# Optimization experiments

Measured on AMD Instinct MI355X. Metric: run time of the kernel, lower is better.

Reference implementation:

```python
import jax, jax.numpy as jnp
import numpy as np

K_HOPS = 2


def setup_inputs() -> dict:
    key = jax.random.key(0)
    k1, k2, k3 = jax.random.split(key, 3)
    N, E, D, C = 100000, 3200000, 512, 40
    x = jax.random.normal(k1, (N, D), dtype=jnp.float32)
    edge_index = jax.random.randint(k2, (2, E), 0, N, dtype=jnp.int64)
    W = jax.random.normal(k3, (C, D), dtype=jnp.float32) * 0.05
    b = jnp.zeros((C,), dtype=jnp.float32)
    return {"x": x, "edge_index": edge_index, "W": W, "b": b}


def reference(x, edge_index, W, b):
    # SGConv: K-hop symmetric-normalized propagation, then Linear, then log_softmax.
    # Dropout is identity at inference (training=False).
    N = x.shape[0]
    loop = jnp.arange(N, dtype=edge_index.dtype)
    src = jnp.concatenate([edge_index[0], loop])  # source nodes (+ self-loops)
    dst = jnp.concatenate([edge_index[1], loop])  # target nodes (+ self-loops)
    ew = jnp.ones(src.shape[0], dtype=x.dtype)
    # deg^{-1/2} A_hat deg^{-1/2}: degree computed at the target (col) index, as in PyG gcn_norm
    deg = jax.ops.segment_sum(ew, dst, num_segments=N)
    dinv = jnp.where(deg > 0, jax.lax.rsqrt(deg), 0.0)
    norm = dinv[src] * dinv[dst]  # [E+N]
    h = x
    for _ in range(K_HOPS):
        # gather source features, weight, scatter-add to targets
        h = jax.ops.segment_sum(norm[:, None] * h[src], dst, num_segments=N)
    logits = h @ W.T + b  # [N, C]
    return jax.nn.log_softmax(logits, axis=1)
```

## Files before the change

### kernel.cpp

```cpp
#include <hip/hip_runtime.h>
#include <hip/hip_bf16.h>


#define TPB 256
#define ETILE 16384
#define ZS 64

typedef __attribute__((ext_vector_type(8))) short short8v;
typedef __attribute__((ext_vector_type(4))) float f32x4;

__device__ inline short f2bf(float f) {
    unsigned u = __float_as_uint(f);
    unsigned r = (u + 0x7fffu + ((u >> 16) & 1u)) >> 16;
    return (short)r;
}
__device__ inline float bf2f(short s) {
    return __uint_as_float(((unsigned)(unsigned short)s) << 16);
}

__global__ void k_wconv(const float* __restrict__ W, short* __restrict__ Wb,
                        int* __restrict__ bcnt, int nb) {
    if (blockIdx.x == 0)
        for (int i = threadIdx.x; i < nb; i += TPB) bcnt[i] = 0;
    int idx = blockIdx.x * TPB + threadIdx.x;
    int c = idx >> 9, k = idx & 511;
    float v = (c < 40) ? W[c * 512 + k] : 0.f;
    Wb[idx] = f2bf(v);
}

__global__ __launch_bounds__(TPB) void k_bhist(
    const int* __restrict__ dst, int* __restrict__ bcnt, int E, int nb) {
    __shared__ int h[512];
    int t = threadIdx.x;
    for (int i = t; i < nb; i += TPB) h[i] = 0;
    __syncthreads();
    int e0 = blockIdx.x * ETILE;
    int e1 = min(e0 + ETILE, E);
    for (int e = e0 + t; e < e1; e += TPB)
        atomicAdd(&h[dst[e] >> 8], 1);
    __syncthreads();
    for (int i = t; i < nb; i += TPB)
        if (h[i]) atomicAdd(&bcnt[i], h[i]);
}

__global__ __launch_bounds__(512) void k_boff(
    const int* __restrict__ bcnt, int* __restrict__ boff,
    int* __restrict__ bcur, int nb) {
    __shared__ int s[512];
    int t = threadIdx.x;
    int own = (t < nb) ? bcnt[t] : 0;
    s[t] = own;
    __syncthreads();
    for (int off = 1; off < 512; off <<= 1) {
        int v = (t >= off) ? s[t - off] : 0;
        __syncthreads();
        s[t] += v;
        __syncthreads();
    }
    if (t < nb) {
        int ex = s[t] - own;
        boff[t] = ex;
        bcur[t] = ex;
        if (t == nb - 1) boff[nb] = s[t];
    }
}

__global__ __launch_bounds__(TPB) void k_part(
    const int* __restrict__ src, const int* __restrict__ dst,
    int* __restrict__ bcur, int* __restrict__ pairs, int E, int nb) {
    __shared__ int hist[512], base[512];
    int t = threadIdx.x;
    for (int i = t; i < nb; i += TPB) hist[i] = 0;
    __syncthreads();
    int e0 = blockIdx.x * ETILE;
    int e1 = min(e0 + ETILE, E);
    for (int e = e0 + t; e < e1; e += TPB)
        atomicAdd(&hist[dst[e] >> 8], 1);
    __syncthreads();
    for (int i = t; i < nb; i += TPB) {
        base[i] = hist[i] ? atomicAdd(&bcur[i], hist[i]) : 0;
        hist[i] = 0;
    }
    __syncthreads();
    for (int e = e0 + t; e < e1; e += TPB) {
        int d = dst[e];
        int b = d >> 8;
        int pos = base[b] + atomicAdd(&hist[b], 1);
        pairs[pos] = ((d & 255) << 20) | src[e];
    }
}

__global__ __launch_bounds__(TPB) void k_sort(
    const int* __restrict__ pairs, const int* __restrict__ boff,
    int* __restrict__ csr, int* __restrict__ row_ptr, float* __restrict__ dinv,
    int N, int nb) {
    __shared__ int hist[256], excl[256], lcur[256];
    int b = blockIdx.x, t = threadIdx.x;
    hist[t] = 0;
    __syncthreads();
    int beg = boff[b], end = boff[b + 1];
    for (int j = beg + t; j < end; j += TPB)
        atomicAdd(&hist[pairs[j] >> 20], 1);
    __syncthreads();
    int own = hist[t];
    excl[t] = own;
    __syncthreads();
    for (int off = 1; off < 256; off <<= 1) {
        int v = (t >= off) ? excl[t - off] : 0;
        __syncthreads();
        excl[t] += v;
        __syncthreads();
    }
    int node = (b << 8) + t;
    if (node < N) {
        row_ptr[node] = beg + excl[t] - own;
        dinv[node] = rsqrtf((float)(own + 1));
    }
    lcur[t] = 0;
    __syncthreads();
    for (int j = beg + t; j < end; j += TPB) {
        int u = pairs[j];
        int dl = u >> 20;
        int pos = beg + (excl[dl] - hist[dl]) + atomicAdd(&lcur[dl], 1);
        csr[pos] = u & 0xFFFFF;
    }
    if (b == nb - 1 && t == 0) row_ptr[N] = end;
}

__global__ __launch_bounds__(TPB) void k_matmul_mfma(
    const float* __restrict__ x, const short* __restrict__ Wb,
    const float* __restrict__ dinv, short* __restrict__ z, int N) {
    int wid  = threadIdx.x >> 6;
    int lane = threadIdx.x & 63;
    int rbase = blockIdx.x * 64 + wid * 16;
    if (rbase >= N) return;
    int arow   = rbase + (lane & 15);
    int aclamp = min(arow, N - 1);
    int koff   = (lane >> 4) * 8;
    const float* xrow = x + (size_t)aclamp * 512 + koff;
    const short* wb   = Wb + (lane & 15) * 512 + koff;

    f32x4 acc0 = {0.f,0.f,0.f,0.f}, acc1 = {0.f,0.f,0.f,0.f}, acc2 = {0.f,0.f,0.f,0.f};
    for (int ks = 0; ks < 16; ++ks) {
        int k0 = ks * 32;
        float4 f0 = *reinterpret_cast<const float4*>(xrow + k0);
        float4 f1 = *reinterpret_cast<const float4*>(xrow + k0 + 4);
        short8v a;
        a[0] = f2bf(f0.x); a[1] = f2bf(f0.y); a[2] = f2bf(f0.z); a[3] = f2bf(f0.w);
        a[4] = f2bf(f1.x); a[5] = f2bf(f1.y); a[6] = f2bf(f1.z); a[7] = f2bf(f1.w);
        short8v b0 = *reinterpret_cast<const short8v*>(wb + k0);
        short8v b1 = *reinterpret_cast<const short8v*>(wb + 16 * 512 + k0);
        short8v b2 = *reinterpret_cast<const short8v*>(wb + 32 * 512 + k0);
        acc0 = __builtin_amdgcn_mfma_f32_16x16x32_bf16(a, b0, acc0, 0, 0, 0);
        acc1 = __builtin_amdgcn_mfma_f32_16x16x32_bf16(a, b1, acc1, 0, 0, 0);
        acc2 = __builtin_amdgcn_mfma_f32_16x16x32_bf16(a, b2, acc2, 0, 0, 0);
    }
    int col = lane & 15;
    int rw  = rbase + (lane >> 4) * 4;
#pragma unroll
    for (int reg = 0; reg < 4; ++reg) {
        int r = rw + reg;
        if (r < N) {
            float di = dinv[r];
            short* zr = z + (size_t)r * ZS;
            zr[col]      = f2bf(di * acc0[reg]);
            zr[16 + col] = f2bf(di * acc1[reg]);
            zr[32 + col] = f2bf(di * acc2[reg]);
            zr[48 + col] = 0;
        }
    }
}

__device__ inline void gather_acc(
    const short8v* __restrict__ Z, const int* __restrict__ csr,
    int beg, int end, int c8, float acc[8]) {
    int j = beg;
    for (; j + 4 <= end; j += 4) {
        int s0 = csr[j], s1 = csr[j+1], s2 = csr[j+2], s3 = csr[j+3];
        short8v v0 = Z[s0 * 8 + c8];
        short8v v1 = Z[s1 * 8 + c8];
        short8v v2 = Z[s2 * 8 + c8];
        short8v v3 = Z[s3 * 8 + c8];
#pragma unroll
        for (int k = 0; k < 8; ++k)
            acc[k] += (bf2f(v0[k]) + bf2f(v1[k])) + (bf2f(v2[k]) + bf2f(v3[k]));
    }
    for (; j < end; ++j) {
        short8v v = Z[csr[j] * 8 + c8];
#pragma unroll
        for (int k = 0; k < 8; ++k) acc[k] += bf2f(v[k]);
    }
}

__global__ __launch_bounds__(TPB) void k_hop1(
    const int* __restrict__ csr, const int* __restrict__ row_ptr,
    const float* __restrict__ dinv, const short* __restrict__ zin,
    short* __restrict__ zout, int N) {
    int t = blockIdx.x * TPB + threadIdx.x;
    int node = t >> 3;
    int c8 = t & 7;
    if (node >= N) return;
    const short8v* Z = reinterpret_cast<const short8v*>(zin);
    short8v sv = Z[node * 8 + c8];
    float acc[8];
#pragma unroll
    for (int k = 0; k < 8; ++k) acc[k] = bf2f(sv[k]);
    gather_acc(Z, csr, row_ptr[node], row_ptr[node + 1], c8, acc);
    float dd = dinv[node];
    float sc = dd * dd;
    short8v o;
#pragma unroll
    for (int k = 0; k < 8; ++k) o[k] = f2bf(sc * acc[k]);
    reinterpret_cast<short8v*>(zout)[node * 8 + c8] = o;
}

__global__ __launch_bounds__(TPB) void k_hop2_lsm(
    const int* __restrict__ csr, const int* __restrict__ row_ptr,
    const float* __restrict__ dinv, const short* __restrict__ zin,
    const float* __restrict__ bias, float* __restrict__ out, int N) {
    int t = blockIdx.x * TPB + threadIdx.x;
    int node = t >> 3;
    int c8 = t & 7;
    if (node >= N) return;
    const short8v* Z = reinterpret_cast<const short8v*>(zin);
    short8v sv = Z[node * 8 + c8];
    float acc[8];
#pragma unroll
    for (int k = 0; k < 8; ++k) acc[k] = bf2f(sv[k]);
    gather_acc(Z, csr, row_ptr[node], row_ptr[node + 1], c8, acc);
    float dd = dinv[node];

    float v[8];
    float lm = -1e30f;
    bool live = (c8 < 5);
    if (live) {
#pragma unroll
        for (int k = 0; k < 8; ++k) {
            v[k] = dd * acc[k] + bias[c8 * 8 + k];
            lm = fmaxf(lm, v[k]);
        }
    }
    float gm = lm;
    gm = fmaxf(gm, __shfl_xor(gm, 1));
    gm = fmaxf(gm, __shfl_xor(gm, 2));
    gm = fmaxf(gm, __shfl_xor(gm, 4));
    float ls = 0.f;
    if (live) {
#pragma unroll
        for (int k = 0; k < 8; ++k) ls += __expf(v[k] - gm);
    }
    ls += __shfl_xor(ls, 1);
    ls += __shfl_xor(ls, 2);
    ls += __shfl_xor(ls, 4);
    if (live) {
        float lse = gm + __logf(ls);
        float* op = out + (size_t)node * 40 + c8 * 8;
        *reinterpret_cast<float4*>(op)     = make_float4(v[0]-lse, v[1]-lse, v[2]-lse, v[3]-lse);
        *reinterpret_cast<float4*>(op + 4) = make_float4(v[4]-lse, v[5]-lse, v[6]-lse, v[7]-lse);
    }
}

extern "C" void kernel_launch(void* const* d_in, const int* in_sizes, int n_in,
                              void* d_out, int out_size, void* d_ws, size_t ws_size,
                              hipStream_t stream) {
    const float* x  = (const float*)d_in[0];
    const int*   ei = (const int*)d_in[1];
    const float* W  = (const float*)d_in[2];
    const float* b  = (const float*)d_in[3];
    float* out = (float*)d_out;

    const int N = in_sizes[0] / 512;
    const int E = in_sizes[1] / 2;
    const int* src = ei;
    const int* dst = ei + E;
    const int nb = (N + 255) >> 8;

    short* z0      = (short*)d_ws;
    short* z1      = z0 + (size_t)N * ZS;
    int*   pairs   = (int*)z1;
    int*   csr     = (int*)(z1 + (size_t)N * ZS);
    int*   bcnt    = csr + E;
    int*   boff    = bcnt + nb;
    int*   bcur    = boff + nb + 1;
    int*   row_ptr = bcur + nb;
    float* dinv    = (float*)(row_ptr + N + 1);
    short* Wb      = (short*)(dinv + N);

    int gT  = (E + ETILE - 1) / ETILE;
    int gM  = (N + 63) / 64;
    int gH  = (N * 8 + TPB - 1) / TPB;

    k_wconv<<<(48 * 512) / TPB, TPB, 0, stream>>>(W, Wb, bcnt, nb);
    k_bhist<<<gT, TPB, 0, stream>>>(dst, bcnt, E, nb);
    k_boff<<<1, 512, 0, stream>>>(bcnt, boff, bcur, nb);
    k_part<<<gT, TPB, 0, stream>>>(src, dst, bcur, pairs, E, nb);
    k_sort<<<nb, TPB, 0, stream>>>(pairs, boff, csr, row_ptr, dinv, N, nb);

    k_matmul_mfma<<<gM, TPB, 0, stream>>>(x, Wb, dinv, z0, N);

    k_hop1<<<gH, TPB, 0, stream>>>(csr, row_ptr, dinv, z0, z1, N);
    k_hop2_lsm<<<gH, TPB, 0, stream>>>(csr, row_ptr, dinv, z1, b, out, N);
}
```

Baseline: 310.7 us.

## Sort nodes by degree within buckets for balanced gather and nontemporal CSR loads

During CSR construction each 256-node bucket is counting-sorted by in-degree (capped at 255), and the result is stored as a permutation. Both hop kernels walk nodes through this permutation so that neighbouring wavefronts process nodes of similar degree, which cuts loop-length divergence inside a wavefront. CSR index loads become nontemporal to keep cache space for the gathered feature rows. The cost is an extra indirection load, scattered output writes within each bucket, and more shared-memory scans in the sort kernel.

```diff
diff --git a/kernel.cpp b/kernel.cpp
--- a/kernel.cpp
+++ b/kernel.cpp
@@ -93,10 +93,10 @@
 __global__ __launch_bounds__(TPB) void k_sort(
     const int* __restrict__ pairs, const int* __restrict__ boff,
     int* __restrict__ csr, int* __restrict__ row_ptr, float* __restrict__ dinv,
-    int N, int nb) {
-    __shared__ int hist[256], excl[256], lcur[256];
+    int* __restrict__ perm, int N, int nb) {
+    __shared__ int hist[256], excl[256], lcur[256], dh[256], dcnt[256];
     int b = blockIdx.x, t = threadIdx.x;
-    hist[t] = 0;
+    hist[t] = 0; dh[t] = 0;
     __syncthreads();
     int beg = boff[b], end = boff[b + 1];
     for (int j = beg + t; j < end; j += TPB)
@@ -112,10 +112,28 @@
         __syncthreads();
     }
     int node = (b << 8) + t;
+    int dv = -1;
     if (node < N) {
         row_ptr[node] = beg + excl[t] - own;
         dinv[node] = rsqrtf((float)(own + 1));
-    }
+        dv = min(own, 255);
+        atomicAdd(&dh[dv], 1);
+    }
+    lcur[t] = 0;
+    __syncthreads();
+    dcnt[t] = dh[t];
+    __syncthreads();
+    for (int off = 1; off < 256; off <<= 1) {
+        int v = (t >= off) ? dh[t - off] : 0;
+        __syncthreads();
+        dh[t] += v;
+        __syncthreads();
+    }
+    if (dv >= 0) {
+        int rank = dh[dv] - dcnt[dv] + atomicAdd(&lcur[dv], 1);
+        perm[(b << 8) + rank] = node;
+    }
+    __syncthreads();
     lcur[t] = 0;
     __syncthreads();
     for (int j = beg + t; j < end; j += TPB) {
@@ -176,7 +194,10 @@
     int beg, int end, int c8, float acc[8]) {
     int j = beg;
     for (; j + 4 <= end; j += 4) {
-        int s0 = csr[j], s1 = csr[j+1], s2 = csr[j+2], s3 = csr[j+3];
+        int s0 = __builtin_nontemporal_load(csr + j);
+        int s1 = __builtin_nontemporal_load(csr + j + 1);
+        int s2 = __builtin_nontemporal_load(csr + j + 2);
+        int s3 = __builtin_nontemporal_load(csr + j + 3);
         short8v v0 = Z[s0 * 8 + c8];
         short8v v1 = Z[s1 * 8 + c8];
         short8v v2 = Z[s2 * 8 + c8];
@@ -186,7 +207,7 @@
             acc[k] += (bf2f(v0[k]) + bf2f(v1[k])) + (bf2f(v2[k]) + bf2f(v3[k]));
     }
     for (; j < end; ++j) {
-        short8v v = Z[csr[j] * 8 + c8];
+        short8v v = Z[__builtin_nontemporal_load(csr + j) * 8 + c8];
 #pragma unroll
         for (int k = 0; k < 8; ++k) acc[k] += bf2f(v[k]);
     }
@@ -194,12 +215,14 @@
 
 __global__ __launch_bounds__(TPB) void k_hop1(
     const int* __restrict__ csr, const int* __restrict__ row_ptr,
+    const int* __restrict__ perm,
     const float* __restrict__ dinv, const short* __restrict__ zin,
     short* __restrict__ zout, int N) {
     int t = blockIdx.x * TPB + threadIdx.x;
-    int node = t >> 3;
+    int gidx = t >> 3;
     int c8 = t & 7;
-    if (node >= N) return;
+    if (gidx >= N) return;
+    int node = perm[gidx];
     const short8v* Z = reinterpret_cast<const short8v*>(zin);
     short8v sv = Z[node * 8 + c8];
     float acc[8];
@@ -216,12 +239,14 @@
 
 __global__ __launch_bounds__(TPB) void k_hop2_lsm(
     const int* __restrict__ csr, const int* __restrict__ row_ptr,
+    const int* __restrict__ perm,
     const float* __restrict__ dinv, const short* __restrict__ zin,
     const float* __restrict__ bias, float* __restrict__ out, int N) {
     int t = blockIdx.x * TPB + threadIdx.x;
-    int node = t >> 3;
+    int gidx = t >> 3;
     int c8 = t & 7;
-    if (node >= N) return;
+    if (gidx >= N) return;
+    int node = perm[gidx];
     const short8v* Z = reinterpret_cast<const short8v*>(zin);
     short8v sv = Z[node * 8 + c8];
     float acc[8];
@@ -285,6 +310,7 @@
     int*   row_ptr = bcur + nb;
     float* dinv    = (float*)(row_ptr + N + 1);
     short* Wb      = (short*)(dinv + N);
+    int*   perm    = (int*)(Wb + 48 * 512);
 
     int gT  = (E + ETILE - 1) / ETILE;
     int gM  = (N + 63) / 64;
@@ -294,10 +320,10 @@
     k_bhist<<<gT, TPB, 0, stream>>>(dst, bcnt, E, nb);
     k_boff<<<1, 512, 0, stream>>>(bcnt, boff, bcur, nb);
     k_part<<<gT, TPB, 0, stream>>>(src, dst, bcur, pairs, E, nb);
-    k_sort<<<nb, TPB, 0, stream>>>(pairs, boff, csr, row_ptr, dinv, N, nb);
+    k_sort<<<nb, TPB, 0, stream>>>(pairs, boff, csr, row_ptr, dinv, perm, N, nb);
 
     k_matmul_mfma<<<gM, TPB, 0, stream>>>(x, Wb, dinv, z0, N);
 
-    k_hop1<<<gH, TPB, 0, stream>>>(csr, row_ptr, dinv, z0, z1, N);
-    k_hop2_lsm<<<gH, TPB, 0, stream>>>(csr, row_ptr, dinv, z1, b, out, N);
-}
+    k_hop1<<<gH, TPB, 0, stream>>>(csr, row_ptr, perm, dinv, z0, z1, N);
+    k_hop2_lsm<<<gH, TPB, 0, stream>>>(csr, row_ptr, perm, dinv, z1, b, out, N);
+}
```

Measured after the change: 353.6 us. 13.8% more time.
